# Optimization experiments

Hardware: AMD Instinct MI355X
Metric: run time of the kernel (lower is better)

The kernel has to match this reference:

```python
import math
import jax, jax.numpy as jnp
import numpy as np

DIM, HEADS, HD = 384, 12, 32
FEAT, WIN, SHIFT = (64, 64), (8, 8), (4, 4)
L = WIN[0] * WIN[1]  # window area = 64
MAX_LOGIT = math.log(1.0 / 0.01)


def _rel_log_coords():
    # pair-wise relative positions, log-spaced (static, numpy)
    coords = np.stack(np.meshgrid(np.arange(WIN[0]), np.arange(WIN[1]), indexing='ij'), 0).reshape(2, -1)
    rel = (coords[:, :, None] - coords[:, None, :]).transpose(1, 2, 0).reshape(-1, 2).astype(np.float32)
    return np.sign(rel) * np.log1p(np.abs(rel))  # [L*L, 2]


def _attn_mask():
    # shifted-window attention mask (static, numpy): 9 regions -> -100 across regions
    H, W = FEAT
    img = np.zeros((H, W), np.int32)
    cnt = 0
    for h0, h1 in ((0, H - WIN[0]), (H - WIN[0], H - SHIFT[0]), (H - SHIFT[0], H)):
        for w0, w1 in ((0, W - WIN[1]), (W - WIN[1], W - SHIFT[1]), (W - SHIFT[1], W)):
            img[h0:h1, w0:w1] = cnt
            cnt += 1
    mw = img.reshape(H // WIN[0], WIN[0], W // WIN[1], WIN[1]).transpose(0, 2, 1, 3).reshape(-1, L)
    diff = mw[:, None, :] - mw[:, :, None]
    return np.where(diff != 0, -100.0, 0.0).astype(np.float32)  # [nW, L, L]


def _ln(x, w, b, eps=1e-5):
    mu = x.mean(-1, keepdims=True)
    var = ((x - mu) ** 2).mean(-1, keepdims=True)
    return (x - mu) / jnp.sqrt(var + eps) * w + b


def setup_inputs() -> dict:
    key = jax.random.key(0)
    ks = jax.random.split(key, 12)
    B = 32
    s = 0.02
    return {
        'x': jax.random.normal(ks[0], (B, FEAT[0], FEAT[1], DIM), jnp.float32),
        'qkv_w': jax.random.normal(ks[1], (3 * DIM, DIM), jnp.float32) * s,
        'qkv_b': jnp.zeros((3 * DIM,), jnp.float32),
        'proj_w': jax.random.normal(ks[2], (DIM, DIM), jnp.float32) * s,
        'proj_b': jnp.zeros((DIM,), jnp.float32),
        'meta_w1': jax.random.normal(ks[3], (384, 2), jnp.float32) * 0.1,
        'meta_b1': jnp.zeros((384,), jnp.float32),
        'meta_w2': jax.random.normal(ks[4], (HEADS, 384), jnp.float32) * 0.1,
        'meta_b2': jnp.zeros((HEADS,), jnp.float32),
        'logit_scale': jnp.full((HEADS,), math.log(10.0), jnp.float32),
        'norm1_w': jnp.ones((DIM,), jnp.float32),
        'norm1_b': jnp.zeros((DIM,), jnp.float32),
        'fc1_w': jax.random.normal(ks[5], (4 * DIM, DIM), jnp.float32) * s,
        'fc1_b': jnp.zeros((4 * DIM,), jnp.float32),
        'fc2_w': jax.random.normal(ks[6], (DIM, 4 * DIM), jnp.float32) * s,
        'fc2_b': jnp.zeros((DIM,), jnp.float32),
        'norm2_w': jnp.ones((DIM,), jnp.float32),
        'norm2_b': jnp.zeros((DIM,), jnp.float32),
    }


def reference(x, qkv_w, qkv_b, proj_w, proj_b, meta_w1, meta_b1, meta_w2, meta_b2,
              logit_scale, norm1_w, norm1_b, fc1_w, fc1_b, fc2_w, fc2_b, norm2_w, norm2_b):
    B, H, W, C = x.shape
    wh, ww = WIN
    # cyclic shift + window partition: (B,H,W,C) -> (B*nW, L, C)
    sx = jnp.roll(x, (-SHIFT[0], -SHIFT[1]), axis=(1, 2))
    xw = sx.reshape(B, H // wh, wh, W // ww, ww, C).transpose(0, 1, 3, 2, 4, 5).reshape(-1, L, C)
    Bw = xw.shape[0]
    qkv = (xw @ qkv_w.T + qkv_b).reshape(Bw, L, 3, HEADS, HD).transpose(2, 0, 3, 1, 4)
    q, k, v = qkv[0], qkv[1], qkv[2]  # [Bw, heads, L, hd]
    # cosine attention
    qn = q / jnp.maximum(jnp.linalg.norm(q, axis=-1, keepdims=True), 1e-12)
    kn = k / jnp.maximum(jnp.linalg.norm(k, axis=-1, keepdims=True), 1e-12)
    attn = jnp.einsum('bhqd,bhkd->bhqk', qn, kn)
    scale = jnp.exp(jnp.minimum(logit_scale, MAX_LOGIT)).reshape(1, HEADS, 1, 1)
    # MLP-based relative position bias
    rel = jnp.asarray(_rel_log_coords())
    bias = jax.nn.relu(rel @ meta_w1.T + meta_b1) @ meta_w2.T + meta_b2  # [L*L, heads]
    bias = bias.T.reshape(HEADS, L, L)
    attn = attn * scale + bias[None]
    # shift mask
    mask = jnp.asarray(_attn_mask())  # [nW, L, L]
    nW = mask.shape[0]
    attn = attn.reshape(Bw // nW, nW, HEADS, L, L) + mask[None, :, None]
    attn = jax.nn.softmax(attn.reshape(Bw, HEADS, L, L), axis=-1)
    out = jnp.einsum('bhqk,bhkd->bhqd', attn, v).transpose(0, 2, 1, 3).reshape(Bw, L, C)
    out = out @ proj_w.T + proj_b
    # window reverse + reverse shift
    out = out.reshape(B, H // wh, W // ww, wh, ww, C).transpose(0, 1, 3, 2, 4, 5).reshape(B, H, W, C)
    out = jnp.roll(out, (SHIFT[0], SHIFT[1]), axis=(1, 2))
    # post-norm residuals (SwinV2Cr style)
    x = x + _ln(out, norm1_w, norm1_b)
    h = jax.nn.gelu(x @ fc1_w.T + fc1_b, approximate=False) @ fc2_w.T + fc2_b
    x = x + _ln(h, norm2_w, norm2_b)
    return x
```

## Files before the change

kernel.cpp:

```cpp
#include <hip/hip_runtime.h>
#include <hip/hip_bf16.h>

typedef __attribute__((ext_vector_type(4))) float f32x4;
typedef __attribute__((ext_vector_type(4))) unsigned int u32x4;
typedef __attribute__((ext_vector_type(8))) __bf16 bf16x8;

#define DEV static __device__ __forceinline__

DEV unsigned short f2bf(float f) {
  unsigned u = __builtin_bit_cast(unsigned, f);
  u += 0x7fffu + ((u >> 16) & 1u);
  return (unsigned short)(u >> 16);
}
DEV float bf2f(unsigned short b) {
  return __builtin_bit_cast(float, ((unsigned)b) << 16);
}
DEV unsigned pk2(float a, float b) {
  return (unsigned)f2bf(a) | ((unsigned)f2bf(b) << 16);
}
DEV unsigned cvtpk(float lo, float hi) {
  unsigned r;
  asm("v_cvt_pk_bf16_f32 %0, %1, %2" : "=v"(r) : "v"(lo), "v"(hi));
  return r;
}
DEV float fexp2(float x) {
  float r;
  asm("v_exp_f32 %0, %1" : "=v"(r) : "v"(x));
  return r;
}
DEV f32x4 mfma16(u32x4 a, u32x4 b, f32x4 c) {
  return __builtin_amdgcn_mfma_f32_16x16x32_bf16(
      __builtin_bit_cast(bf16x8, a), __builtin_bit_cast(bf16x8, b), c, 0, 0, 0);
}
DEV float ssq8(u32x4 c) {
  float s = 0.f;
#pragma unroll
  for (int e = 0; e < 4; e++) {
    float lo = __builtin_bit_cast(float, c[e] << 16);
    float hi = __builtin_bit_cast(float, c[e] & 0xffff0000u);
    s += lo * lo + hi * hi;
  }
  return s;
}
DEV void gload16(const unsigned short* g, unsigned short* l) {
  __builtin_amdgcn_global_load_lds(
      (const __attribute__((address_space(1))) unsigned int*)g,
      (__attribute__((address_space(3))) unsigned int*)l, 16, 0, 0);
}

template <int EPI>
__global__ __launch_bounds__(512, 2) void gemm8(
    const unsigned short* __restrict__ A, const unsigned short* __restrict__ B,
    const float* __restrict__ bias, unsigned short* __restrict__ C,
    int Nld, int K, int nblocks) {
  __shared__ __align__(16) unsigned short As[2][256 * 64];
  __shared__ __align__(16) unsigned short Bs[2][256 * 64];
  const int bid = blockIdx.x;
  const int mchunk = (gridDim.x >> 3) / nblocks;
  const int xcd = bid & 7, idx = bid >> 3;
  const int nb = idx % nblocks, ml = idx / nblocks;
  const int m0 = (xcd * mchunk + ml) * 256, n0 = nb * 256;
  const int tid = threadIdx.x, w = tid >> 6, l = tid & 63;
  const int lr = l & 15, lg = l >> 4;
  const int wm = (w >> 2) * 128, wn = (w & 3) * 64;
  const int srow = l >> 3;
  const int scol = ((l & 7) ^ srow) * 8;
  const int NT = K >> 6;

  auto stA = [&](int p, int kt, int half, int j) {
    int r = half * 128 + w * 16 + j * 8;
    gload16(A + (size_t)(m0 + r + srow) * K + kt * 64 + scol, &As[p][r * 64]);
  };
  auto stB = [&](int p, int kt, int half, int j) {
    int r = half * 128 + w * 16 + j * 8;
    gload16(B + (size_t)(n0 + r + srow) * K + kt * 64 + scol, &Bs[p][r * 64]);
  };

  const f32x4 z4 = {0.f, 0.f, 0.f, 0.f};
  f32x4 acc[8][4];
#pragma unroll
  for (int i = 0; i < 8; i++)
#pragma unroll
    for (int j = 0; j < 4; j++) acc[i][j] = z4;
  u32x4 af[8], bf[8];

#pragma unroll
  for (int ktp = 0; ktp < 2; ktp++) {
    stB(ktp, ktp, 0, 0); stB(ktp, ktp, 0, 1);
    stB(ktp, ktp, 1, 0); stB(ktp, ktp, 1, 1);
    stA(ktp, ktp, 0, 0); stA(ktp, ktp, 0, 1);
    stA(ktp, ktp, 1, 0); stA(ktp, ktp, 1, 1);
  }

  for (int kt = 0; kt < NT; ++kt) {
    const int p = kt & 1;
    if (kt + 1 < NT) {
      asm volatile("s_waitcnt vmcnt(8)" ::: "memory");
    } else {
      asm volatile("s_waitcnt vmcnt(0)" ::: "memory");
    }
    __builtin_amdgcn_s_barrier();

#pragma unroll
    for (int ni = 0; ni < 4; ni++)
#pragma unroll
      for (int ks = 0; ks < 2; ks++) {
        int R = wn + ni * 16 + lr;
        bf[ni * 2 + ks] =
            *(const u32x4*)&Bs[p][R * 64 + (((ks * 4 + lg) ^ (lr & 7)) * 8)];
      }
#pragma unroll
    for (int mi = 0; mi < 4; mi++)
#pragma unroll
      for (int ks = 0; ks < 2; ks++) {
        int R = wm + mi * 16 + lr;
        af[mi * 2 + ks] =
            *(const u32x4*)&As[p][R * 64 + (((ks * 4 + lg) ^ (lr & 7)) * 8)];
      }
    asm volatile("s_waitcnt lgkmcnt(0)" ::: "memory");
    __builtin_amdgcn_sched_barrier(0);
    __builtin_amdgcn_s_setprio(1);
#pragma unroll
    for (int mi = 0; mi < 4; mi++)
#pragma unroll
      for (int ni = 0; ni < 2; ni++)
#pragma unroll
        for (int ks = 0; ks < 2; ks++)
          acc[mi][ni] = mfma16(af[mi * 2 + ks], bf[ni * 2 + ks], acc[mi][ni]);
    __builtin_amdgcn_s_setprio(0);
    __builtin_amdgcn_s_barrier();

    if (kt + 2 < NT) { stB(p, kt + 2, 0, 0); stB(p, kt + 2, 0, 1); }
    __builtin_amdgcn_s_setprio(1);
#pragma unroll
    for (int mi = 0; mi < 4; mi++)
#pragma unroll
      for (int ni = 0; ni < 2; ni++)
#pragma unroll
        for (int ks = 0; ks < 2; ks++)
          acc[mi][ni + 2] =
              mfma16(af[mi * 2 + ks], bf[(ni + 2) * 2 + ks], acc[mi][ni + 2]);
    __builtin_amdgcn_s_setprio(0);
    __builtin_amdgcn_s_barrier();

#pragma unroll
    for (int mi = 0; mi < 4; mi++)
#pragma unroll
      for (int ks = 0; ks < 2; ks++) {
        int R = wm + 64 + mi * 16 + lr;
        af[mi * 2 + ks] =
            *(const u32x4*)&As[p][R * 64 + (((ks * 4 + lg) ^ (lr & 7)) * 8)];
      }
    if (kt + 2 < NT) { stB(p, kt + 2, 1, 0); stB(p, kt + 2, 1, 1); }
    asm volatile("s_waitcnt lgkmcnt(0)" ::: "memory");
    __builtin_amdgcn_sched_barrier(0);
    __builtin_amdgcn_s_setprio(1);
#pragma unroll
    for (int mi = 0; mi < 4; mi++)
#pragma unroll
      for (int ni = 0; ni < 2; ni++)
#pragma unroll
        for (int ks = 0; ks < 2; ks++)
          acc[mi + 4][ni] =
              mfma16(af[mi * 2 + ks], bf[ni * 2 + ks], acc[mi + 4][ni]);
    __builtin_amdgcn_s_setprio(0);
    __builtin_amdgcn_s_barrier();

    if (kt + 2 < NT) {
      stA(p, kt + 2, 0, 0); stA(p, kt + 2, 0, 1);
      stA(p, kt + 2, 1, 0); stA(p, kt + 2, 1, 1);
    }
    __builtin_amdgcn_s_setprio(1);
#pragma unroll
    for (int mi = 0; mi < 4; mi++)
#pragma unroll
      for (int ni = 0; ni < 2; ni++)
#pragma unroll
        for (int ks = 0; ks < 2; ks++)
          acc[mi + 4][ni + 2] =
              mfma16(af[mi * 2 + ks], bf[(ni + 2) * 2 + ks], acc[mi + 4][ni + 2]);
    __builtin_amdgcn_s_setprio(0);
  }

#pragma unroll
  for (int ni = 0; ni < 4; ni++) {
    int ncol = n0 + wn + ni * 16 + lr;
    float bv = bias[ncol];
#pragma unroll
    for (int mh = 0; mh < 2; mh++)
#pragma unroll
      for (int mi = 0; mi < 4; mi++) {
        int mbase = m0 + wm + mh * 64 + mi * 16 + lg * 4;
#pragma unroll
        for (int r = 0; r < 4; r++) {
          float v = acc[mh * 4 + mi][ni][r] + bv;
          if (EPI == 1) v = 0.5f * v * (1.0f + erff(v * 0.70710678f));
          C[(size_t)(mbase + r) * Nld + ncol] = f2bf(v);
        }
      }
  }
}

template <int MODE>
__global__ __launch_bounds__(512) void gemm_ln(
    const unsigned short* __restrict__ A, const unsigned short* __restrict__ Bw,
    const float* __restrict__ bias, const float* __restrict__ resf,
    const unsigned short* __restrict__ resb, const float* __restrict__ nw,
    const float* __restrict__ nb, unsigned short* __restrict__ outb,
    float* __restrict__ outf, int K) {
  __shared__ __align__(16) unsigned short As[2][4096];
  __shared__ __align__(16) unsigned short Bs[2][12288];
  const int bid = blockIdx.x;
  const int swz = (bid & 7) * (gridDim.x >> 3) + (bid >> 3);
  const int m0 = swz * 128;
  const int tid = threadIdx.x, w8 = tid >> 6, l = tid & 63;
  const int lr = l & 15, lg = l >> 4;
  const int gsw = (lg ^ ((lr >> 1) & 3)) * 8;
  const int wm2 = (w8 >> 2) * 64;
  const int wn4 = w8 & 3;

  const int rs = l >> 2;
  const int gsrc = ((l & 3) ^ ((l >> 3) & 3)) * 8;
  const unsigned short* g_src[4];
  unsigned short* g_dst[4];
  int g_str[4];
#pragma unroll
  for (int i = 0; i < 4; i++) {
    int g = w8 * 4 + i;
    if (g < 8) {
      g_src[i] = A + (size_t)(m0 + g * 16 + rs) * K + gsrc;
      g_dst[i] = &As[0][g * 512];
      g_str[i] = 4096;
    } else {
      g_src[i] = Bw + (size_t)((g - 8) * 16 + rs) * K + gsrc;
      g_dst[i] = &Bs[0][(g - 8) * 512];
      g_str[i] = 12288;
    }
  }
  auto stage = [&](int buf, int k0) {
#pragma unroll
    for (int i = 0; i < 4; i++) gload16(g_src[i] + k0, g_dst[i] + buf * g_str[i]);
  };

  const f32x4 z4 = {0.f, 0.f, 0.f, 0.f};
  f32x4 acc[4][6];
#pragma unroll
  for (int i = 0; i < 4; i++)
#pragma unroll
    for (int j = 0; j < 6; j++) acc[i][j] = z4;

  auto compute = [&](int buf) {
    u32x4 a[4], b[6];
#pragma unroll
    for (int i = 0; i < 4; i++)
      a[i] = *(const u32x4*)(&As[buf][(wm2 + i * 16 + lr) * 32 + gsw]);
#pragma unroll
    for (int j = 0; j < 6; j++)
      b[j] = *(const u32x4*)(&Bs[buf][(wn4 * 96 + j * 16 + lr) * 32 + gsw]);
#pragma unroll
    for (int i = 0; i < 4; i++)
#pragma unroll
      for (int j = 0; j < 6; j++) acc[i][j] = mfma16(a[i], b[j], acc[i][j]);
  };

  const int nt = K >> 5;
  stage(0, 0);
  for (int t = 0; t < nt; ++t) {
    __syncthreads();
    if (t + 1 < nt) stage((t + 1) & 1, (t + 1) * 32);
    compute(t & 1);
  }

  float bcol[6];
#pragma unroll
  for (int j = 0; j < 6; j++) bcol[j] = bias[wn4 * 96 + j * 16 + lr];
#pragma unroll
  for (int i = 0; i < 4; i++)
#pragma unroll
    for (int j = 0; j < 6; j++)
#pragma unroll
      for (int r = 0; r < 4; r++) acc[i][j][r] += bcol[j];

  float* psum = (float*)(&As[0][0]);
  float* psq  = (float*)(&As[0][1024]);
#pragma unroll
  for (int i = 0; i < 4; i++)
#pragma unroll
    for (int r = 0; r < 4; r++) {
      float s1 = 0.f, s2 = 0.f;
#pragma unroll
      for (int j = 0; j < 6; j++) {
        float v = acc[i][j][r];
        s1 += v;
        s2 += v * v;
      }
#pragma unroll
      for (int d = 1; d < 16; d <<= 1) {
        s1 += __shfl_xor(s1, d, 64);
        s2 += __shfl_xor(s2, d, 64);
      }
      if (lr == 0) {
        int row = wm2 + i * 16 + lg * 4 + r;
        psum[wn4 * 128 + row] = s1;
        psq[wn4 * 128 + row] = s2;
      }
    }
  __syncthreads();

  float wcol[6], b2col[6];
#pragma unroll
  for (int j = 0; j < 6; j++) {
    int col = wn4 * 96 + j * 16 + lr;
    wcol[j] = nw[col];
    b2col[j] = nb[col];
  }
#pragma unroll
  for (int i = 0; i < 4; i++)
#pragma unroll
    for (int r = 0; r < 4; r++) {
      int row = wm2 + i * 16 + lg * 4 + r;
      float sum = psum[row] + psum[128 + row] + psum[256 + row] + psum[384 + row];
      float sq = psq[row] + psq[128 + row] + psq[256 + row] + psq[384 + row];
      float mu = sum * (1.f / 384.f);
      float rstd = rsqrtf(sq * (1.f / 384.f) - mu * mu + 1e-5f);
      size_t nbase;
      if (MODE == 0) {
        int mrow = m0 + row;
        int bb = mrow >> 12, widx = (mrow >> 6) & 63, tt = mrow & 63;
        int yy = (((widx >> 3) << 3) + (tt >> 3) + 4) & 63;
        int xx = (((widx & 7) << 3) + (tt & 7) + 4) & 63;
        nbase = (size_t)((bb << 12) | (yy << 6) | xx) * 384;
      } else {
        nbase = (size_t)(m0 + row) * 384;
      }
#pragma unroll
      for (int j = 0; j < 6; j++) {
        int col = wn4 * 96 + j * 16 + lr;
        float v = (acc[i][j][r] - mu) * rstd * wcol[j] + b2col[j];
        if (MODE == 0) {
          outb[nbase + col] = f2bf(resf[nbase + col] + v);
        } else {
          outf[nbase + col] = bf2f(resb[nbase + col]) + v;
        }
      }
    }
}

__global__ __launch_bounds__(256) void gather_cvt(
    const float* __restrict__ x, unsigned short* __restrict__ xb) {
  int wv = threadIdx.x >> 6, l = threadIdx.x & 63;
  int m = blockIdx.x * 4 + wv;
  int w = m >> 6, t = m & 63;
  int b = w >> 6, wy = (w >> 3) & 7, wx = w & 7;
  int oy = (wy * 8 + (t >> 3) + 4) & 63;
  int ox = (wx * 8 + (t & 7) + 4) & 63;
  const float2* src =
      (const float2*)(x + (size_t)((((b << 6) | oy) << 6) | ox) * 384 + l * 6);
  float2 f0 = src[0], f1 = src[1], f2 = src[2];
  unsigned* dst = (unsigned*)(xb + (size_t)m * 384 + l * 6);
  dst[0] = pk2(f0.x, f0.y);
  dst[1] = pk2(f1.x, f1.y);
  dst[2] = pk2(f2.x, f2.y);
}

__global__ __launch_bounds__(256, 4) void attn_win(
    const unsigned short* __restrict__ qkv, const float* __restrict__ btab2,
    const float* __restrict__ lscale, unsigned short* __restrict__ aout) {
  __shared__ __align__(16) unsigned short vT[4][32 * 72];
  __shared__ __align__(16) float rnk[4][64];
  const int w = blockIdx.x;
  const int wv = threadIdx.x >> 6, l = threadIdx.x & 63;
  const int h = blockIdx.y * 4 + wv;
  const int lr = l & 15, lg = l >> 4;
  const size_t base = (size_t)w * 64 * 1280 + h * 32;
  const f32x4 z4 = {0.f, 0.f, 0.f, 0.f};

  {
    const u32x4* vp = (const u32x4*)(qkv + base + (size_t)l * 1280 + 768);
#pragma unroll
    for (int c4 = 0; c4 < 4; c4++) {
      u32x4 c = vp[c4];
#pragma unroll
      for (int e = 0; e < 4; e++) {
        vT[wv][(c4 * 8 + e * 2) * 72 + l] = (unsigned short)(c[e] & 0xffffu);
        vT[wv][(c4 * 8 + e * 2 + 1) * 72 + l] = (unsigned short)(c[e] >> 16);
      }
    }
  }
  u32x4 kf[4];
#pragma unroll
  for (int tj = 0; tj < 4; tj++) {
    kf[tj] = *(const u32x4*)(qkv + base + (size_t)(tj * 16 + lr) * 1280 + 384 + lg * 8);
    float s = ssq8(kf[tj]);
    s += __shfl_xor(s, 16, 64);
    s += __shfl_xor(s, 32, 64);
    if (lg == 0) rnk[wv][tj * 16 + lr] = rsqrtf(fmaxf(s, 1e-24f));
  }
  u32x4 qf[4];
  float rnq[4];
#pragma unroll
  for (int ti = 0; ti < 4; ti++) {
    qf[ti] = *(const u32x4*)(qkv + base + (size_t)(ti * 16 + lr) * 1280 + lg * 8);
    float s = ssq8(qf[ti]);
    s += __shfl_xor(s, 16, 64);
    s += __shfl_xor(s, 32, 64);
    rnq[ti] = rsqrtf(fmaxf(s, 1e-24f));
  }
  __syncthreads();

  u32x4 vb[2][2];
#pragma unroll
  for (int kc = 0; kc < 2; kc++)
#pragma unroll
    for (int tj2 = 0; tj2 < 2; tj2++)
      vb[kc][tj2] = *(const u32x4*)(&vT[wv][(tj2 * 16 + lr) * 72 + kc * 32 + lg * 8]);

  const float scl2 = expf(fminf(lscale[h], 4.6051702f)) * 1.44269504f;
  const int wt = ((((w >> 3) & 7) == 7) ? 2 : 0) | (((w & 7) == 7) ? 1 : 0);
  const float* tabh = btab2 + (((size_t)wt * 12 + h) << 12);
  const int s0l = lr + ((l & 16) ? 32 : 0);
  const int s1l = s0l + 16;
  const bool hi = (l & 32) != 0;

#pragma unroll
  for (int ti = 0; ti < 4; ti++) {
    f32x4 sv[4];
#pragma unroll
    for (int tj = 0; tj < 4; tj++) sv[tj] = mfma16(kf[tj], qf[ti], z4);
    const float* tab = tabh + ((ti * 16 + lr) << 6);
    const float cb = rnq[ti] * scl2;
    f32x4 val[4];
    float m = -1e30f;
#pragma unroll
    for (int tj = 0; tj < 4; tj++) {
      f32x4 rk4 = *(const f32x4*)(&rnk[wv][tj * 16 + lg * 4]);
      f32x4 t4 = *(const f32x4*)(tab + tj * 16 + lg * 4);
#pragma unroll
      for (int r = 0; r < 4; r++) {
        float v = sv[tj][r] * (cb * rk4[r]) + t4[r];
        val[tj][r] = v;
        m = fmaxf(m, v);
      }
    }
    m = fmaxf(m, __shfl_xor(m, 16, 64));
    m = fmaxf(m, __shfl_xor(m, 32, 64));
    float den = 0.f;
#pragma unroll
    for (int tj = 0; tj < 4; tj++)
#pragma unroll
      for (int r = 0; r < 4; r++) {
        float p = fexp2(val[tj][r] - m);
        val[tj][r] = p;
        den += p;
      }
    den += __shfl_xor(den, 16, 64);
    den += __shfl_xor(den, 32, 64);
    float rden = 1.f / den;
#pragma unroll
    for (int tj = 0; tj < 4; tj++)
#pragma unroll
      for (int r = 0; r < 4; r++) val[tj][r] *= rden;

    f32x4 o[2] = {z4, z4};
#pragma unroll
    for (int kc = 0; kc < 2; kc++) {
      unsigned yA0 = cvtpk(val[2 * kc][0], val[2 * kc][1]);
      unsigned yA1 = cvtpk(val[2 * kc][2], val[2 * kc][3]);
      unsigned yB0 = cvtpk(val[2 * kc + 1][0], val[2 * kc + 1][1]);
      unsigned yB1 = cvtpk(val[2 * kc + 1][2], val[2 * kc + 1][3]);
      unsigned a0 = __shfl((int)yA0, s0l, 64), b0 = __shfl((int)yB0, s0l, 64);
      unsigned a1 = __shfl((int)yA1, s0l, 64), b1 = __shfl((int)yB1, s0l, 64);
      unsigned a2 = __shfl((int)yA0, s1l, 64), b2 = __shfl((int)yB0, s1l, 64);
      unsigned a3 = __shfl((int)yA1, s1l, 64), b3 = __shfl((int)yB1, s1l, 64);
      u32x4 pa = {hi ? b0 : a0, hi ? b1 : a1, hi ? b2 : a2, hi ? b3 : a3};
#pragma unroll
      for (int tj2 = 0; tj2 < 2; tj2++) o[tj2] = mfma16(pa, vb[kc][tj2], o[tj2]);
    }
#pragma unroll
    for (int tj2 = 0; tj2 < 2; tj2++)
#pragma unroll
      for (int r = 0; r < 4; r++)
        aout[(size_t)(w * 64 + ti * 16 + lg * 4 + r) * 384 + h * 32 + tj2 * 16 + lr] =
            f2bf(o[tj2][r]);
  }
}

__global__ __launch_bounds__(256) void btab2_kernel(
    const float* __restrict__ w1, const float* __restrict__ b1,
    const float* __restrict__ w2, const float* __restrict__ b2,
    float* __restrict__ btab2) {
  int p = blockIdx.x * 256 + threadIdx.x;
  int i = p >> 6, j = p & 63;
  float dy = (float)((i >> 3) - (j >> 3));
  float dx = (float)((i & 7) - (j & 7));
  float r0 = (dy > 0.f ? 1.f : (dy < 0.f ? -1.f : 0.f)) * log1pf(fabsf(dy));
  float r1 = (dx > 0.f ? 1.f : (dx < 0.f ? -1.f : 0.f)) * log1pf(fabsf(dx));
  float acc[12];
#pragma unroll
  for (int hh = 0; hh < 12; hh++) acc[hh] = b2[hh];
  for (int c = 0; c < 384; c++) {
    float hv = w1[c * 2] * r0 + w1[c * 2 + 1] * r1 + b1[c];
    hv = fmaxf(hv, 0.f);
#pragma unroll
    for (int hh = 0; hh < 12; hh++) acc[hh] += hv * w2[hh * 384 + c];
  }
  bool ddy = ((i >> 3) >= 4) != ((j >> 3) >= 4);
  bool ddx = ((i & 7) >= 4) != ((j & 7) >= 4);
  const float L2E = 1.44269504f;
#pragma unroll
  for (int wt = 0; wt < 4; wt++) {
    float mask = ((((wt >> 1) != 0) && ddy) || (((wt & 1) != 0) && ddx)) ? -100.f : 0.f;
#pragma unroll
    for (int hh = 0; hh < 12; hh++)
      btab2[(((size_t)wt * 12 + hh) << 12) + p] = (acc[hh] + mask) * L2E;
  }
}

__global__ __launch_bounds__(256) void cvt_kernel(
    const float* __restrict__ s, unsigned short* __restrict__ d, int n) {
  int i = blockIdx.x * 256 + threadIdx.x;
  if (i < n) d[i] = f2bf(s[i]);
}

__global__ __launch_bounds__(256) void cvt_pad_kernel(
    const float* __restrict__ s, unsigned short* __restrict__ d, int n_src,
    int n_tot) {
  int i = blockIdx.x * 256 + threadIdx.x;
  if (i < n_tot) d[i] = (i < n_src) ? f2bf(s[i]) : (unsigned short)0;
}

__global__ __launch_bounds__(256) void pad_bias_kernel(
    const float* __restrict__ s, float* __restrict__ d) {
  int i = blockIdx.x * 256 + threadIdx.x;
  if (i < 1280) d[i] = (i < 1152) ? s[i] : 0.f;
}

extern "C" void kernel_launch(void* const* d_in, const int* in_sizes, int n_in,
                              void* d_out, int out_size, void* d_ws,
                              size_t ws_size, hipStream_t stream) {
  (void)in_sizes; (void)n_in; (void)out_size; (void)ws_size;
  const float* x      = (const float*)d_in[0];
  const float* qkv_w  = (const float*)d_in[1];
  const float* qkv_b  = (const float*)d_in[2];
  const float* proj_w = (const float*)d_in[3];
  const float* proj_b = (const float*)d_in[4];
  const float* mw1    = (const float*)d_in[5];
  const float* mb1    = (const float*)d_in[6];
  const float* mw2    = (const float*)d_in[7];
  const float* mb2    = (const float*)d_in[8];
  const float* lsc    = (const float*)d_in[9];
  const float* n1w    = (const float*)d_in[10];
  const float* n1b    = (const float*)d_in[11];
  const float* w1     = (const float*)d_in[12];
  const float* b1     = (const float*)d_in[13];
  const float* w2     = (const float*)d_in[14];
  const float* b2     = (const float*)d_in[15];
  const float* n2w    = (const float*)d_in[16];
  const float* n2b    = (const float*)d_in[17];

  char* ws = (char*)d_ws;
  unsigned short* wqb  = (unsigned short*)(ws + 0);
  unsigned short* wpb  = (unsigned short*)(ws + 1048576);
  unsigned short* w1b  = (unsigned short*)(ws + 1441792);
  unsigned short* w2b  = (unsigned short*)(ws + 2621440);
  float* qbp           = (float*)(ws + 3801088);
  float* btab2         = (float*)(ws + 3866624);
  unsigned short* xb   = (unsigned short*)(ws + 4718592);
  unsigned short* qkvb = (unsigned short*)(ws + 105381888);
  unsigned short* att  = (unsigned short*)(ws + 440926208);
  unsigned short* hb   = (unsigned short*)(ws + 541589504);
  unsigned short* y1b  = xb;
  float* yout = (float*)d_out;

  cvt_pad_kernel<<<dim3(1920), 256, 0, stream>>>(qkv_w, wqb, 442368, 491520);
  cvt_kernel<<<dim3(576), 256, 0, stream>>>(proj_w, wpb, 147456);
  cvt_kernel<<<dim3(2304), 256, 0, stream>>>(w1, w1b, 589824);
  cvt_kernel<<<dim3(2304), 256, 0, stream>>>(w2, w2b, 589824);
  pad_bias_kernel<<<dim3(5), 256, 0, stream>>>(qkv_b, qbp);
  btab2_kernel<<<dim3(16), 256, 0, stream>>>(mw1, mb1, mw2, mb2, btab2);
  gather_cvt<<<dim3(32768), 256, 0, stream>>>(x, xb);

  gemm8<0><<<dim3(2560), 512, 0, stream>>>(xb, wqb, qbp, qkvb, 1280, 384, 5);
  attn_win<<<dim3(2048, 3), 256, 0, stream>>>(qkvb, btab2, lsc, att);
  gemm_ln<0><<<dim3(1024), 512, 0, stream>>>(
      att, wpb, proj_b, x, nullptr, n1w, n1b, y1b, nullptr, 384);
  for (int c = 0; c < 4; c++) {
    const unsigned short* ya = y1b + (size_t)c * 32768 * 384;
    float* yc = yout + (size_t)c * 32768 * 384;
    gemm8<1><<<dim3(768), 512, 0, stream>>>(ya, w1b, b1, hb, 1536, 384, 6);
    gemm_ln<1><<<dim3(256), 512, 0, stream>>>(
        hb, w2b, b2, nullptr, ya, n2w, n2b, nullptr, yc, 1536);
  }
}
```

Before: 1.287 ms.

## Stage GEMM epilogue through LDS for coalesced stores and drop QKV padding

Swaps the MFMA operand order so each lane holds four consecutive output columns. The GEMM epilogue then writes packed bf16 results into a swizzled shared-memory tile and stores them to global memory as coalesced 16-byte rows, replacing scattered 2-byte stores. The QKV output stride shrinks from the padded 1280 columns to 1152, with padded columns skipped, which cuts write and read traffic between the QKV GEMM and attention. The change adds an LDS round trip and barriers at the end of every GEMM tile.

New measurement: 1.192 ms. 1.08x faster.

```diff
diff --git a/kernel.cpp b/kernel.cpp
--- a/kernel.cpp
+++ b/kernel.cpp
@@ -52,9 +52,10 @@
 __global__ __launch_bounds__(512, 2) void gemm8(
     const unsigned short* __restrict__ A, const unsigned short* __restrict__ B,
     const float* __restrict__ bias, unsigned short* __restrict__ C,
-    int Nld, int K, int nblocks) {
-  __shared__ __align__(16) unsigned short As[2][256 * 64];
-  __shared__ __align__(16) unsigned short Bs[2][256 * 64];
+    int Nc, int K, int nblocks) {
+  __shared__ __align__(16) unsigned char smem[131072];
+  unsigned short* As0 = (unsigned short*)smem;
+  unsigned short* Bs0 = (unsigned short*)(smem + 65536);
   const int bid = blockIdx.x;
   const int mchunk = (gridDim.x >> 3) / nblocks;
   const int xcd = bid & 7, idx = bid >> 3;
@@ -69,11 +70,13 @@
 
   auto stA = [&](int p, int kt, int half, int j) {
     int r = half * 128 + w * 16 + j * 8;
-    gload16(A + (size_t)(m0 + r + srow) * K + kt * 64 + scol, &As[p][r * 64]);
+    gload16(A + (size_t)(m0 + r + srow) * K + kt * 64 + scol,
+            As0 + p * 16384 + r * 64);
   };
   auto stB = [&](int p, int kt, int half, int j) {
     int r = half * 128 + w * 16 + j * 8;
-    gload16(B + (size_t)(n0 + r + srow) * K + kt * 64 + scol, &Bs[p][r * 64]);
+    gload16(B + (size_t)(n0 + r + srow) * K + kt * 64 + scol,
+            Bs0 + p * 16384 + r * 64);
   };
 
   const f32x4 z4 = {0.f, 0.f, 0.f, 0.f};
@@ -106,16 +109,16 @@
 #pragma unroll
       for (int ks = 0; ks < 2; ks++) {
         int R = wn + ni * 16 + lr;
-        bf[ni * 2 + ks] =
-            *(const u32x4*)&Bs[p][R * 64 + (((ks * 4 + lg) ^ (lr & 7)) * 8)];
+        bf[ni * 2 + ks] = *(const u32x4*)&Bs0[p * 16384 + R * 64 +
+                                             (((ks * 4 + lg) ^ (lr & 7)) * 8)];
       }
 #pragma unroll
     for (int mi = 0; mi < 4; mi++)
 #pragma unroll
       for (int ks = 0; ks < 2; ks++) {
         int R = wm + mi * 16 + lr;
-        af[mi * 2 + ks] =
-            *(const u32x4*)&As[p][R * 64 + (((ks * 4 + lg) ^ (lr & 7)) * 8)];
+        af[mi * 2 + ks] = *(const u32x4*)&As0[p * 16384 + R * 64 +
+                                              (((ks * 4 + lg) ^ (lr & 7)) * 8)];
       }
     asm volatile("s_waitcnt lgkmcnt(0)" ::: "memory");
     __builtin_amdgcn_sched_barrier(0);
@@ -126,7 +129,7 @@
       for (int ni = 0; ni < 2; ni++)
 #pragma unroll
         for (int ks = 0; ks < 2; ks++)
-          acc[mi][ni] = mfma16(af[mi * 2 + ks], bf[ni * 2 + ks], acc[mi][ni]);
+          acc[mi][ni] = mfma16(bf[ni * 2 + ks], af[mi * 2 + ks], acc[mi][ni]);
     __builtin_amdgcn_s_setprio(0);
     __builtin_amdgcn_s_barrier();
 
@@ -139,7 +142,7 @@
 #pragma unroll
         for (int ks = 0; ks < 2; ks++)
           acc[mi][ni + 2] =
-              mfma16(af[mi * 2 + ks], bf[(ni + 2) * 2 + ks], acc[mi][ni + 2]);
+              mfma16(bf[(ni + 2) * 2 + ks], af[mi * 2 + ks], acc[mi][ni + 2]);
     __builtin_amdgcn_s_setprio(0);
     __builtin_amdgcn_s_barrier();
 
@@ -148,8 +151,8 @@
 #pragma unroll
       for (int ks = 0; ks < 2; ks++) {
         int R = wm + 64 + mi * 16 + lr;
-        af[mi * 2 + ks] =
-            *(const u32x4*)&As[p][R * 64 + (((ks * 4 + lg) ^ (lr & 7)) * 8)];
+        af[mi * 2 + ks] = *(const u32x4*)&As0[p * 16384 + R * 64 +
+                                              (((ks * 4 + lg) ^ (lr & 7)) * 8)];
       }
     if (kt + 2 < NT) { stB(p, kt + 2, 1, 0); stB(p, kt + 2, 1, 1); }
     asm volatile("s_waitcnt lgkmcnt(0)" ::: "memory");
@@ -162,7 +165,7 @@
 #pragma unroll
         for (int ks = 0; ks < 2; ks++)
           acc[mi + 4][ni] =
-              mfma16(af[mi * 2 + ks], bf[ni * 2 + ks], acc[mi + 4][ni]);
+              mfma16(bf[ni * 2 + ks], af[mi * 2 + ks], acc[mi + 4][ni]);
     __builtin_amdgcn_s_setprio(0);
     __builtin_amdgcn_s_barrier();
 
@@ -178,26 +181,40 @@
 #pragma unroll
         for (int ks = 0; ks < 2; ks++)
           acc[mi + 4][ni + 2] =
-              mfma16(af[mi * 2 + ks], bf[(ni + 2) * 2 + ks], acc[mi + 4][ni + 2]);
+              mfma16(bf[(ni + 2) * 2 + ks], af[mi * 2 + ks], acc[mi + 4][ni + 2]);
     __builtin_amdgcn_s_setprio(0);
   }
 
-#pragma unroll
-  for (int ni = 0; ni < 4; ni++) {
-    int ncol = n0 + wn + ni * 16 + lr;
-    float bv = bias[ncol];
-#pragma unroll
-    for (int mh = 0; mh < 2; mh++)
-#pragma unroll
-      for (int mi = 0; mi < 4; mi++) {
-        int mbase = m0 + wm + mh * 64 + mi * 16 + lg * 4;
+  __builtin_amdgcn_s_barrier();
+#pragma unroll
+  for (int mh = 0; mh < 2; mh++)
+#pragma unroll
+    for (int mi = 0; mi < 4; mi++) {
+      int mloc = wm + mh * 64 + mi * 16 + lr;
+      int msw = mloc & 7;
+#pragma unroll
+      for (int ni = 0; ni < 4; ni++) {
+        f32x4 v = acc[mh * 4 + mi][ni];
+        f32x4 bv = *(const f32x4*)&bias[n0 + wn + ni * 16 + lg * 4];
 #pragma unroll
         for (int r = 0; r < 4; r++) {
-          float v = acc[mh * 4 + mi][ni][r] + bv;
-          if (EPI == 1) v = 0.5f * v * (1.0f + erff(v * 0.70710678f));
-          C[(size_t)(mbase + r) * Nld + ncol] = f2bf(v);
+          float t = v[r] + bv[r];
+          if (EPI == 1) t = 0.5f * t * (1.0f + erff(t * 0.70710678f));
+          v[r] = t;
         }
-      }
+        int nbyte = (wn + ni * 16 + lg * 4) * 2;
+        int addr = mloc * 512 + ((((nbyte >> 4) ^ msw) << 4) | (nbyte & 8));
+        *(uint2*)(smem + addr) = make_uint2(cvtpk(v[0], v[1]), cvtpk(v[2], v[3]));
+      }
+    }
+  __syncthreads();
+#pragma unroll
+  for (int c = 0; c < 16; c++) {
+    int m = w * 32 + c * 2 + (l >> 5);
+    int h = l & 31;
+    u32x4 v = *(const u32x4*)(smem + m * 512 + ((h ^ (m & 7)) << 4));
+    int n = n0 + h * 8;
+    if (n < Nc) *(u32x4*)&C[(size_t)(m0 + m) * Nc + n] = v;
   }
 }
 
@@ -372,11 +389,11 @@
   const int wv = threadIdx.x >> 6, l = threadIdx.x & 63;
   const int h = blockIdx.y * 4 + wv;
   const int lr = l & 15, lg = l >> 4;
-  const size_t base = (size_t)w * 64 * 1280 + h * 32;
+  const size_t base = (size_t)w * 64 * 1152 + h * 32;
   const f32x4 z4 = {0.f, 0.f, 0.f, 0.f};
 
   {
-    const u32x4* vp = (const u32x4*)(qkv + base + (size_t)l * 1280 + 768);
+    const u32x4* vp = (const u32x4*)(qkv + base + (size_t)l * 1152 + 768);
 #pragma unroll
     for (int c4 = 0; c4 < 4; c4++) {
       u32x4 c = vp[c4];
@@ -390,7 +407,7 @@
   u32x4 kf[4];
 #pragma unroll
   for (int tj = 0; tj < 4; tj++) {
-    kf[tj] = *(const u32x4*)(qkv + base + (size_t)(tj * 16 + lr) * 1280 + 384 + lg * 8);
+    kf[tj] = *(const u32x4*)(qkv + base + (size_t)(tj * 16 + lr) * 1152 + 384 + lg * 8);
     float s = ssq8(kf[tj]);
     s += __shfl_xor(s, 16, 64);
     s += __shfl_xor(s, 32, 64);
@@ -400,7 +417,7 @@
   float rnq[4];
 #pragma unroll
   for (int ti = 0; ti < 4; ti++) {
-    qf[ti] = *(const u32x4*)(qkv + base + (size_t)(ti * 16 + lr) * 1280 + lg * 8);
+    qf[ti] = *(const u32x4*)(qkv + base + (size_t)(ti * 16 + lr) * 1152 + lg * 8);
     float s = ssq8(qf[ti]);
     s += __shfl_xor(s, 16, 64);
     s += __shfl_xor(s, 32, 64);
@@ -580,7 +597,7 @@
   btab2_kernel<<<dim3(16), 256, 0, stream>>>(mw1, mb1, mw2, mb2, btab2);
   gather_cvt<<<dim3(32768), 256, 0, stream>>>(x, xb);
 
-  gemm8<0><<<dim3(2560), 512, 0, stream>>>(xb, wqb, qbp, qkvb, 1280, 384, 5);
+  gemm8<0><<<dim3(2560), 512, 0, stream>>>(xb, wqb, qbp, qkvb, 1152, 384, 5);
   attn_win<<<dim3(2048, 3), 256, 0, stream>>>(qkvb, btab2, lsc, att);
   gemm_ln<0><<<dim3(1024), 512, 0, stream>>>(
       att, wpb, proj_b, x, nullptr, n1w, n1b, y1b, nullptr, 384);
```
